# Optimization experiments

Measured on AMD Instinct MI355X. Metric: run time of the kernel, lower is better.

## Reference

```python
import jax, jax.numpy as jnp
import numpy as np

N_NODES = 100000
N_EDGES = 1280000
D_IN = 64
D_HID = 128
D_OUT = 64


def sage_conv(x, src, dst, W_l, b_l, W_r, n_nodes):
    # PyG SAGEConv (aggr='mean', root_weight=True):
    #   out_i = W_l @ mean_{j in N(i)} x_j + b_l + W_r @ x_i
    msg = x[src]  # [E, d] gather of source-node features
    agg = jax.ops.segment_sum(msg, dst, num_segments=n_nodes)  # [N, d]
    cnt = jax.ops.segment_sum(jnp.ones((src.shape[0], 1), x.dtype), dst,
                              num_segments=n_nodes)  # [N, 1]
    mean = agg / jnp.maximum(cnt, 1.0)  # zero-neighbor nodes -> 0 (matches scatter-mean)
    return mean @ W_l.T + b_l + x @ W_r.T


def setup_inputs() -> dict:
    key = jax.random.key(0)
    ks = jax.random.split(key, 8)
    x = jax.random.normal(ks[0], (N_NODES, D_IN), dtype=jnp.float32)
    edge_index = jax.random.randint(ks[1], (2, N_EDGES), 0, N_NODES, dtype=jnp.int64)
    s = 0.05
    W_l1 = jax.random.normal(ks[2], (D_HID, D_IN), dtype=jnp.float32) * s
    b_l1 = jnp.zeros((D_HID,), dtype=jnp.float32)
    W_r1 = jax.random.normal(ks[3], (D_HID, D_IN), dtype=jnp.float32) * s
    W_l2 = jax.random.normal(ks[4], (D_OUT, D_HID), dtype=jnp.float32) * s
    b_l2 = jnp.zeros((D_OUT,), dtype=jnp.float32)
    W_r2 = jax.random.normal(ks[5], (D_OUT, D_HID), dtype=jnp.float32) * s
    return {"x": x, "edge_index": edge_index,
            "W_l1": W_l1, "b_l1": b_l1, "W_r1": W_r1,
            "W_l2": W_l2, "b_l2": b_l2, "W_r2": W_r2}


def reference(x, edge_index, W_l1, b_l1, W_r1, W_l2, b_l2, W_r2):
    src, dst = edge_index[0], edge_index[1]
    n = x.shape[0]
    h = sage_conv(x, src, dst, W_l1, b_l1, W_r1, n)
    h = jax.nn.relu(h)
    out = sage_conv(h, src, dst, W_l2, b_l2, W_r2, n)
    return out
```

## Files before the change

kernel.cpp:

```cpp
#include <hip/hip_runtime.h>
#include <cstdint>
#include <cstddef>

typedef __attribute__((ext_vector_type(8))) short short8;
typedef __attribute__((ext_vector_type(4))) float floatx4;

static constexpr int DIN  = 64;
static constexpr int DHID = 128;
static constexpr int BSH  = 7;
static constexpr int BNODES = 1 << BSH;
static constexpr int TILE = 8192;
static constexpr int CAP  = 4096;
static constexpr unsigned SENT = 0xFFFFFFFFu;

__device__ inline short f2bf(float f) {
  unsigned u = __float_as_uint(f);
  u += 0x7FFF + ((u >> 16) & 1);
  return (short)(u >> 16);
}
__device__ inline float bf2f(short s) {
  return __uint_as_float(((unsigned)(unsigned short)s) << 16);
}

__global__ __launch_bounds__(64) void detect_kernel(const void* edges, int E, long long nmax, int* mode) {
  const long long* e64 = (const long long*)edges;
  int lane = threadIdx.x;
  int nchk = E < 256 ? E : 256;
  bool ok = true;
  for (int i = lane; i < nchk; i += 64) {
    long long v = e64[i];
    if (v < 0 || v >= nmax) ok = false;
  }
  unsigned long long b = __ballot(ok);
  if (lane == 0) *mode = (b == ~0ull) ? 1 : 0;
}

__global__ __launch_bounds__(256) void prep_kernel(const float* __restrict__ x,
    const float* __restrict__ Wl1, const float* __restrict__ Wr1,
    const float* __restrict__ Wl2, const float* __restrict__ Wr2,
    short* __restrict__ xb, short* __restrict__ wc1, short* __restrict__ wc2,
    int nx, int gx)
{
  int b = blockIdx.x, t = threadIdx.x;
  if (b < gx) {
    int i0 = (b * 256 + t) * 8;
    if (i0 < nx) {
      floatx4 f0 = *(const floatx4*)&x[i0];
      floatx4 f1 = *(const floatx4*)&x[i0 + 4];
      short8 o;
      o[0]=f2bf(f0[0]); o[1]=f2bf(f0[1]); o[2]=f2bf(f0[2]); o[3]=f2bf(f0[3]);
      o[4]=f2bf(f1[0]); o[5]=f2bf(f1[1]); o[6]=f2bf(f1[2]); o[7]=f2bf(f1[3]);
      *(short8*)&xb[i0] = o;
    }
  } else {
    int wb = b - gx;
    int idx = ((wb & 15) * 256 + t) * 4;
    int n = idx >> 7, k = idx & 127;
    const float* src;
    if (wb < 16) src = (k < 64) ? &Wl1[n * 64 + k] : &Wr1[n * 64 + (k - 64)];
    else         src = (n < 64) ? &Wl2[n * 128 + k] : &Wr2[(n - 64) * 128 + k];
    floatx4 f = *(const floatx4*)src;
    short* dst = (wb < 16 ? wc1 : wc2) + idx;
    dst[0]=f2bf(f[0]); dst[1]=f2bf(f[1]); dst[2]=f2bf(f[2]); dst[3]=f2bf(f[3]);
  }
}

__global__ __launch_bounds__(256) void partition_kernel(const void* edges, const int* __restrict__ mode,
                                                        int* __restrict__ bucket_cursor,
                                                        int* __restrict__ real_cnt,
                                                        unsigned* __restrict__ packed, int E, int NB) {
  __shared__ unsigned sval[TILE];
  __shared__ unsigned saux[TILE];
  __shared__ int hist[1024];
  __shared__ int gb[1024];
  int t = threadIdx.x;
  int base = blockIdx.x * TILE;
  int cnt_here = E - base; if (cnt_here > TILE) cnt_here = TILE;
  for (int i = t; i < NB; i += 256) hist[i] = 0;
  __syncthreads();
  bool m64 = (*mode != 0);
  #pragma unroll 4
  for (int c = 0; c < TILE / 256; ++c) {
    int idx = c * 256 + t;
    if (idx < cnt_here) {
      int i = base + idx;
      int s, d;
      if (m64) { const long long* e = (const long long*)edges; s = (int)e[i]; d = (int)e[(size_t)E + i]; }
      else     { const int*       e = (const int*)edges;       s = e[i];      d = e[(size_t)E + i]; }
      int b = d >> BSH;
      int rank = atomicAdd(&hist[b], 1);
      sval[idx] = ((unsigned)(d & (BNODES - 1)) << 17) | (unsigned)s;
      saux[idx] = ((unsigned)b << 13) | (unsigned)rank;
    }
  }
  __syncthreads();
  for (int b = t; b < NB; b += 256) {
    int cnt = hist[b];
    int gbase = 0;
    if (cnt > 0) {
      int pad = (cnt + 15) & ~15;
      gbase = b * CAP + atomicAdd(&bucket_cursor[b], pad);
      atomicAdd(&real_cnt[b], cnt);
      for (int j = cnt; j < pad; ++j) packed[gbase + j] = SENT;
    }
    gb[b] = gbase;
  }
  __syncthreads();
  #pragma unroll 4
  for (int c = 0; c < TILE / 256; ++c) {
    int idx = c * 256 + t;
    if (idx < cnt_here) {
      unsigned a = saux[idx];
      packed[gb[a >> 13] + (a & 0x1FFFu)] = sval[idx];
    }
  }
}

__global__ __launch_bounds__(256) void bucket_scan_kernel(const int* __restrict__ real_cnt,
                                                          int* __restrict__ ebase,
                                                          int* __restrict__ row_ptr,
                                                          int NB, int N, int E) {
  int t = threadIdx.x;
  int i0 = t * 4;
  int v[4]; int s = 0;
  #pragma unroll
  for (int c = 0; c < 4; ++c) { int idx = i0 + c; v[c] = (idx < NB) ? real_cnt[idx] : 0; s += v[c]; }
  int lane = t & 63, w = t >> 6;
  int val = s;
  #pragma unroll
  for (int off = 1; off < 64; off <<= 1) {
    int u = __shfl_up(val, off, 64);
    if (lane >= off) val += u;
  }
  __shared__ int wsum[4];
  if (lane == 63) wsum[w] = val;
  __syncthreads();
  int wpre = 0;
  for (int ww = 0; ww < w; ++ww) wpre += wsum[ww];
  int run = wpre + val - s;
  #pragma unroll
  for (int c = 0; c < 4; ++c) { int idx = i0 + c; if (idx < NB) ebase[idx] = run; run += v[c]; }
  if (t == 0) row_ptr[N] = E;
}

__global__ __launch_bounds__(256) void bucket_sort_kernel(const unsigned* __restrict__ packed,
                                                          const int* __restrict__ bucket_cursor,
                                                          const int* __restrict__ ebase,
                                                          int* __restrict__ row_ptr,
                                                          int* __restrict__ sorted_src, int N) {
  __shared__ int nhist[BNODES];
  __shared__ int cur[BNODES];
  __shared__ int wsum[4];
  int b = blockIdx.x, t = threadIdx.x;
  int n0 = b << BSH;
  int nn = N - n0; if (nn > BNODES) nn = BNODES;
  if (t < BNODES) nhist[t] = 0;
  __syncthreads();
  int rbeg = b * CAP, rcnt = bucket_cursor[b];
  for (int i = t; i < rcnt; i += 256) {
    unsigned p = packed[rbeg + i];
    if (p != SENT) atomicAdd(&nhist[p >> 17], 1);
  }
  __syncthreads();
  int lane = t & 63, w = t >> 6;
  int v = (t < BNODES) ? nhist[t] : 0;
  int val = v;
  #pragma unroll
  for (int off = 1; off < 64; off <<= 1) {
    int u = __shfl_up(val, off, 64);
    if (lane >= off) val += u;
  }
  if (lane == 63) wsum[w] = val;
  __syncthreads();
  int pre = (w == 1) ? wsum[0] : 0;
  int excl = pre + val - v;
  int eb = ebase[b];
  if (t < nn) { row_ptr[n0 + t] = eb + excl; cur[t] = eb + excl; }
  __syncthreads();
  for (int i = t; i < rcnt; i += 256) {
    unsigned p = packed[rbeg + i];
    if (p != SENT) {
      int pos = atomicAdd(&cur[p >> 17], 1);
      sorted_src[pos] = (int)(p & 0x1FFFFu);
    }
  }
}

template <bool EPI>
__global__ __launch_bounds__(256) void agg_bf16_kernel(const short* __restrict__ feat,
                                                       const int* __restrict__ row_ptr,
                                                       const int* __restrict__ srcs,
                                                       const float* __restrict__ rbuf,
                                                       const float* __restrict__ bias,
                                                       short* __restrict__ outb,
                                                       float* __restrict__ outf, int N) {
  int node = blockIdx.x * 32 + (threadIdx.x >> 3);
  if (node >= N) return;
  int c = threadIdx.x & 7;
  const short* fbase = feat + c * 8;
  int beg = row_ptr[node], end = row_ptr[node + 1];
  float acc[8];
  #pragma unroll
  for (int j = 0; j < 8; ++j) acc[j] = 0.f;
  int e = beg;
  for (; e + 4 <= end; e += 4) {
    int s0 = srcs[e], s1 = srcs[e + 1], s2 = srcs[e + 2], s3 = srcs[e + 3];
    short8 v0 = *(const short8*)&fbase[(size_t)s0 * 64];
    short8 v1 = *(const short8*)&fbase[(size_t)s1 * 64];
    short8 v2 = *(const short8*)&fbase[(size_t)s2 * 64];
    short8 v3 = *(const short8*)&fbase[(size_t)s3 * 64];
    #pragma unroll
    for (int j = 0; j < 8; ++j)
      acc[j] += (bf2f(v0[j]) + bf2f(v1[j])) + (bf2f(v2[j]) + bf2f(v3[j]));
  }
  for (; e < end; ++e) {
    short8 v = *(const short8*)&fbase[(size_t)srcs[e] * 64];
    #pragma unroll
    for (int j = 0; j < 8; ++j) acc[j] += bf2f(v[j]);
  }
  float inv = 1.f / fmaxf((float)(end - beg), 1.f);
  if (!EPI) {
    short8 o;
    #pragma unroll
    for (int j = 0; j < 8; ++j) o[j] = f2bf(acc[j] * inv);
    *(short8*)&outb[(size_t)node * 64 + c * 8] = o;
  } else {
    floatx4 b0 = *(const floatx4*)&bias[c * 8];
    floatx4 b1 = *(const floatx4*)&bias[c * 8 + 4];
    floatx4 r0 = *(const floatx4*)&rbuf[(size_t)node * 64 + c * 8];
    floatx4 r1 = *(const floatx4*)&rbuf[(size_t)node * 64 + c * 8 + 4];
    floatx4 o0, o1;
    #pragma unroll
    for (int j = 0; j < 4; ++j) {
      o0[j] = acc[j] * inv + b0[j] + r0[j];
      o1[j] = acc[4 + j] * inv + b1[j] + r1[j];
    }
    *(floatx4*)&outf[(size_t)node * 64 + c * 8]     = o0;
    *(floatx4*)&outf[(size_t)node * 64 + c * 8 + 4] = o1;
  }
}

template <int MODE>
__global__ __launch_bounds__(256) void mfma_gemm_kernel(
    const short* __restrict__ Aa, const short* __restrict__ Ab, int lda,
    const short* __restrict__ Wcat, const float* __restrict__ bias,
    short* __restrict__ Cb, float* __restrict__ Cf, int M)
{
  __shared__ short Ws[128][136];
  int t = threadIdx.x;
  #pragma unroll
  for (int i = 0; i < 8; ++i) {
    int idx = i * 256 + t;
    int r = idx >> 4, c8 = (idx & 15) * 8;
    *(short8*)&Ws[r][c8] = *(const short8*)&Wcat[r * 128 + c8];
  }
  __syncthreads();
  int wv = t >> 6, lane = t & 63, q = lane >> 4, l15 = lane & 15;
  int m0 = blockIdx.x * 64 + wv * 16;
  int row = m0 + l15;
  bool rowok = row < M;
  floatx4 acc[8];
  #pragma unroll
  for (int nt = 0; nt < 8; ++nt) acc[nt] = (floatx4){0.f, 0.f, 0.f, 0.f};
  #pragma unroll
  for (int ko = 0; ko < 4; ++ko) {
    const short* Asrc = (ko < 2) ? Aa : Ab;
    short8 a = {0, 0, 0, 0, 0, 0, 0, 0};
    if (rowok) a = *(const short8*)&Asrc[(size_t)row * lda + (ko & 1) * 32 + q * 8];
    #pragma unroll
    for (int nt = 0; nt < 8; ++nt) {
      short8 b = *(const short8*)&Ws[nt * 16 + l15][ko * 32 + q * 8];
      acc[nt] = __builtin_amdgcn_mfma_f32_16x16x32_bf16(a, b, acc[nt], 0, 0, 0);
    }
  }
  #pragma unroll
  for (int nt = 0; nt < 8; ++nt) {
    int n = nt * 16 + l15;
    float bv = (MODE == 0) ? bias[n] : 0.f;
    #pragma unroll
    for (int r2 = 0; r2 < 4; ++r2) {
      int mr = m0 + q * 4 + r2;
      if (mr >= M) continue;
      float v = acc[nt][r2] + bv;
      if (MODE == 0) {
        v = fmaxf(v, 0.f);
        Cb[(size_t)mr * 128 + n] = f2bf(v);
      } else {
        if (nt < 4) Cb[(size_t)mr * 64 + n] = f2bf(v);
        else        Cf[(size_t)mr * 64 + (n - 64)] = v;
      }
    }
  }
}

extern "C" void kernel_launch(void* const* d_in, const int* in_sizes, int n_in,
                              void* d_out, int out_size, void* d_ws, size_t ws_size,
                              hipStream_t stream) {
  const float* x   = (const float*)d_in[0];
  const void*  ei  = d_in[1];
  const float* Wl1 = (const float*)d_in[2];
  const float* bl1 = (const float*)d_in[3];
  const float* Wr1 = (const float*)d_in[4];
  const float* Wl2 = (const float*)d_in[5];
  const float* bl2 = (const float*)d_in[6];
  const float* Wr2 = (const float*)d_in[7];
  int N = in_sizes[0] / DIN;
  int E = in_sizes[1] / 2;
  int NB = (N + BNODES - 1) / BNODES;

  char* w = (char*)d_ws;
  size_t off = 0;
  auto alloc = [&](size_t bytes) -> void* {
    void* p = w + off;
    off += (bytes + 255) & ~(size_t)255;
    return p;
  };
  int*      mode       = (int*)alloc(16);
  int*      bcur       = (int*)alloc((size_t)NB * 8);
  int*      rcnt       = bcur + NB;
  int*      ebase      = (int*)alloc((size_t)NB * 4);
  int*      row_ptr    = (int*)alloc(((size_t)N + 1) * 4);
  unsigned* packed     = (unsigned*)alloc((size_t)NB * CAP * 4);
  int*      sorted_src = (int*)alloc((size_t)E * 4);
  short*    xb         = (short*)alloc((size_t)N * 64 * 2);
  short*    meanb      = (short*)alloc((size_t)N * 64 * 2);
  short*    h          = (short*)alloc((size_t)N * DHID * 2);
  float*    rbuf       = (float*)alloc((size_t)N * 64 * 4);
  short*    wc1        = (short*)alloc(128 * 128 * 2);
  short*    wc2        = (short*)alloc(128 * 128 * 2);
  (void)ws_size; (void)n_in; (void)out_size;

  hipMemsetAsync(bcur, 0, (size_t)NB * 8, stream);
  detect_kernel<<<1, 64, 0, stream>>>(ei, E, (long long)N, mode);

  int nx = N * DIN;
  int gx = (nx / 8 + 255) / 256;
  prep_kernel<<<gx + 32, 256, 0, stream>>>(x, Wl1, Wr1, Wl2, Wr2, xb, wc1, wc2, nx, gx);

  int gP = (E + TILE - 1) / TILE;
  partition_kernel<<<gP, 256, 0, stream>>>(ei, mode, bcur, rcnt, packed, E, NB);
  bucket_scan_kernel<<<1, 256, 0, stream>>>(rcnt, ebase, row_ptr, NB, N, E);
  bucket_sort_kernel<<<NB, 256, 0, stream>>>(packed, bcur, ebase, row_ptr, sorted_src, N);

  int gN32 = (N + 31) / 32;
  agg_bf16_kernel<false><<<gN32, 256, 0, stream>>>(xb, row_ptr, sorted_src, nullptr, nullptr, meanb, nullptr, N);

  int gm = (N + 63) / 64;
  mfma_gemm_kernel<0><<<gm, 256, 0, stream>>>(meanb, xb, 64, wc1, bl1, h, nullptr, N);
  mfma_gemm_kernel<1><<<gm, 256, 0, stream>>>(h, h + 64, 128, wc2, nullptr, meanb, rbuf, N);

  agg_bf16_kernel<true><<<gN32, 256, 0, stream>>>(meanb, row_ptr, sorted_src, rbuf, bl2, nullptr, (float*)d_out, N);
}
```

Baseline: 222.2 us.

## Fuse both node GEMMs via LDS and fold memset/detect into other kernels

The two MFMA GEMM launches are merged into one kernel. The ReLU'd hidden tile stays in shared memory and feeds the second GEMM directly, so the N×128 bf16 hidden buffer is never written to or read back from global memory. The bucket-cursor memset moves into extra blocks of the prep kernel, and the int64/int32 edge-format check moves into every partition block, removing two small launches. The cost is more LDS per block (second weight load plus the H tile), a redundant format check in each partition block, and the second GEMM's output writing over meanb in place.

Result: faster. 207.4 us (-6.7%).

```diff
diff --git a/kernel.cpp b/kernel.cpp
--- a/kernel.cpp
+++ b/kernel.cpp
@@ -22,23 +22,11 @@
   return __uint_as_float(((unsigned)(unsigned short)s) << 16);
 }
 
-__global__ __launch_bounds__(64) void detect_kernel(const void* edges, int E, long long nmax, int* mode) {
-  const long long* e64 = (const long long*)edges;
-  int lane = threadIdx.x;
-  int nchk = E < 256 ? E : 256;
-  bool ok = true;
-  for (int i = lane; i < nchk; i += 64) {
-    long long v = e64[i];
-    if (v < 0 || v >= nmax) ok = false;
-  }
-  unsigned long long b = __ballot(ok);
-  if (lane == 0) *mode = (b == ~0ull) ? 1 : 0;
-}
-
 __global__ __launch_bounds__(256) void prep_kernel(const float* __restrict__ x,
     const float* __restrict__ Wl1, const float* __restrict__ Wr1,
     const float* __restrict__ Wl2, const float* __restrict__ Wr2,
     short* __restrict__ xb, short* __restrict__ wc1, short* __restrict__ wc2,
+    int* __restrict__ bcur, int nz,
     int nx, int gx)
 {
   int b = blockIdx.x, t = threadIdx.x;
@@ -52,7 +40,7 @@
       o[4]=f2bf(f1[0]); o[5]=f2bf(f1[1]); o[6]=f2bf(f1[2]); o[7]=f2bf(f1[3]);
       *(short8*)&xb[i0] = o;
     }
-  } else {
+  } else if (b < gx + 32) {
     int wb = b - gx;
     int idx = ((wb & 15) * 256 + t) * 4;
     int n = idx >> 7, k = idx & 127;
@@ -62,10 +50,12 @@
     floatx4 f = *(const floatx4*)src;
     short* dst = (wb < 16 ? wc1 : wc2) + idx;
     dst[0]=f2bf(f[0]); dst[1]=f2bf(f[1]); dst[2]=f2bf(f[2]); dst[3]=f2bf(f[3]);
-  }
-}
-
-__global__ __launch_bounds__(256) void partition_kernel(const void* edges, const int* __restrict__ mode,
+  } else {
+    for (int i = t; i < nz; i += 256) bcur[i] = 0;
+  }
+}
+
+__global__ __launch_bounds__(256) void partition_kernel(const void* edges, long long nmax,
                                                         int* __restrict__ bucket_cursor,
                                                         int* __restrict__ real_cnt,
                                                         unsigned* __restrict__ packed, int E, int NB) {
@@ -73,12 +63,25 @@
   __shared__ unsigned saux[TILE];
   __shared__ int hist[1024];
   __shared__ int gb[1024];
+  __shared__ int smode;
   int t = threadIdx.x;
   int base = blockIdx.x * TILE;
   int cnt_here = E - base; if (cnt_here > TILE) cnt_here = TILE;
   for (int i = t; i < NB; i += 256) hist[i] = 0;
-  __syncthreads();
-  bool m64 = (*mode != 0);
+  if (t == 0) smode = 1;
+  __syncthreads();
+  {
+    const long long* e64 = (const long long*)edges;
+    int nchk = E < 256 ? E : 256;
+    bool ok = true;
+    for (int i = t; i < nchk; i += 256) {
+      long long v = e64[i];
+      if (v < 0 || v >= nmax) ok = false;
+    }
+    if (!ok) smode = 0;
+  }
+  __syncthreads();
+  bool m64 = (smode != 0);
   #pragma unroll 4
   for (int c = 0; c < TILE / 256; ++c) {
     int idx = c * 256 + t;
@@ -240,19 +243,20 @@
   }
 }
 
-template <int MODE>
-__global__ __launch_bounds__(256) void mfma_gemm_kernel(
-    const short* __restrict__ Aa, const short* __restrict__ Ab, int lda,
-    const short* __restrict__ Wcat, const float* __restrict__ bias,
-    short* __restrict__ Cb, float* __restrict__ Cf, int M)
+__global__ __launch_bounds__(256) void fused_gemm_kernel(
+    const short* __restrict__ Aa, const short* __restrict__ Ab,
+    const short* __restrict__ wc1, const short* __restrict__ wc2,
+    const float* __restrict__ bias1,
+    short* __restrict__ Cg, float* __restrict__ Cr, int M)
 {
   __shared__ short Ws[128][136];
+  __shared__ short Hs[64][136];
   int t = threadIdx.x;
   #pragma unroll
   for (int i = 0; i < 8; ++i) {
     int idx = i * 256 + t;
     int r = idx >> 4, c8 = (idx & 15) * 8;
-    *(short8*)&Ws[r][c8] = *(const short8*)&Wcat[r * 128 + c8];
+    *(short8*)&Ws[r][c8] = *(const short8*)&wc1[r * 128 + c8];
   }
   __syncthreads();
   int wv = t >> 6, lane = t & 63, q = lane >> 4, l15 = lane & 15;
@@ -266,7 +270,7 @@
   for (int ko = 0; ko < 4; ++ko) {
     const short* Asrc = (ko < 2) ? Aa : Ab;
     short8 a = {0, 0, 0, 0, 0, 0, 0, 0};
-    if (rowok) a = *(const short8*)&Asrc[(size_t)row * lda + (ko & 1) * 32 + q * 8];
+    if (rowok) a = *(const short8*)&Asrc[(size_t)row * 64 + (ko & 1) * 32 + q * 8];
     #pragma unroll
     for (int nt = 0; nt < 8; ++nt) {
       short8 b = *(const short8*)&Ws[nt * 16 + l15][ko * 32 + q * 8];
@@ -276,19 +280,43 @@
   #pragma unroll
   for (int nt = 0; nt < 8; ++nt) {
     int n = nt * 16 + l15;
-    float bv = (MODE == 0) ? bias[n] : 0.f;
+    float bv = bias1[n];
+    #pragma unroll
+    for (int r2 = 0; r2 < 4; ++r2) {
+      int lr = wv * 16 + q * 4 + r2;
+      float v = fmaxf(acc[nt][r2] + bv, 0.f);
+      Hs[lr][n] = f2bf(v);
+    }
+  }
+  __syncthreads();
+  #pragma unroll
+  for (int i = 0; i < 8; ++i) {
+    int idx = i * 256 + t;
+    int r = idx >> 4, c8 = (idx & 15) * 8;
+    *(short8*)&Ws[r][c8] = *(const short8*)&wc2[r * 128 + c8];
+  }
+  __syncthreads();
+  #pragma unroll
+  for (int nt = 0; nt < 8; ++nt) acc[nt] = (floatx4){0.f, 0.f, 0.f, 0.f};
+  #pragma unroll
+  for (int ko = 0; ko < 4; ++ko) {
+    short8 a = *(const short8*)&Hs[wv * 16 + l15][ko * 32 + q * 8];
+    #pragma unroll
+    for (int nt = 0; nt < 8; ++nt) {
+      short8 b = *(const short8*)&Ws[nt * 16 + l15][ko * 32 + q * 8];
+      acc[nt] = __builtin_amdgcn_mfma_f32_16x16x32_bf16(a, b, acc[nt], 0, 0, 0);
+    }
+  }
+  #pragma unroll
+  for (int nt = 0; nt < 8; ++nt) {
+    int n = nt * 16 + l15;
     #pragma unroll
     for (int r2 = 0; r2 < 4; ++r2) {
       int mr = m0 + q * 4 + r2;
       if (mr >= M) continue;
-      float v = acc[nt][r2] + bv;
-      if (MODE == 0) {
-        v = fmaxf(v, 0.f);
-        Cb[(size_t)mr * 128 + n] = f2bf(v);
-      } else {
-        if (nt < 4) Cb[(size_t)mr * 64 + n] = f2bf(v);
-        else        Cf[(size_t)mr * 64 + (n - 64)] = v;
-      }
+      float v = acc[nt][r2];
+      if (nt < 4) Cg[(size_t)mr * 64 + n] = f2bf(v);
+      else        Cr[(size_t)mr * 64 + (n - 64)] = v;
     }
   }
 }
@@ -315,7 +343,6 @@
     off += (bytes + 255) & ~(size_t)255;
     return p;
   };
-  int*      mode       = (int*)alloc(16);
   int*      bcur       = (int*)alloc((size_t)NB * 8);
   int*      rcnt       = bcur + NB;
   int*      ebase      = (int*)alloc((size_t)NB * 4);
@@ -324,21 +351,18 @@
   int*      sorted_src = (int*)alloc((size_t)E * 4);
   short*    xb         = (short*)alloc((size_t)N * 64 * 2);
   short*    meanb      = (short*)alloc((size_t)N * 64 * 2);
-  short*    h          = (short*)alloc((size_t)N * DHID * 2);
   float*    rbuf       = (float*)alloc((size_t)N * 64 * 4);
   short*    wc1        = (short*)alloc(128 * 128 * 2);
   short*    wc2        = (short*)alloc(128 * 128 * 2);
   (void)ws_size; (void)n_in; (void)out_size;
 
-  hipMemsetAsync(bcur, 0, (size_t)NB * 8, stream);
-  detect_kernel<<<1, 64, 0, stream>>>(ei, E, (long long)N, mode);
-
   int nx = N * DIN;
   int gx = (nx / 8 + 255) / 256;
-  prep_kernel<<<gx + 32, 256, 0, stream>>>(x, Wl1, Wr1, Wl2, Wr2, xb, wc1, wc2, nx, gx);
+  prep_kernel<<<gx + 33, 256, 0, stream>>>(x, Wl1, Wr1, Wl2, Wr2, xb, wc1, wc2,
+                                           bcur, NB * 2, nx, gx);
 
   int gP = (E + TILE - 1) / TILE;
-  partition_kernel<<<gP, 256, 0, stream>>>(ei, mode, bcur, rcnt, packed, E, NB);
+  partition_kernel<<<gP, 256, 0, stream>>>(ei, (long long)N, bcur, rcnt, packed, E, NB);
   bucket_scan_kernel<<<1, 256, 0, stream>>>(rcnt, ebase, row_ptr, NB, N, E);
   bucket_sort_kernel<<<NB, 256, 0, stream>>>(packed, bcur, ebase, row_ptr, sorted_src, N);
 
@@ -346,8 +370,7 @@
   agg_bf16_kernel<false><<<gN32, 256, 0, stream>>>(xb, row_ptr, sorted_src, nullptr, nullptr, meanb, nullptr, N);
 
   int gm = (N + 63) / 64;
-  mfma_gemm_kernel<0><<<gm, 256, 0, stream>>>(meanb, xb, 64, wc1, bl1, h, nullptr, N);
-  mfma_gemm_kernel<1><<<gm, 256, 0, stream>>>(h, h + 64, 128, wc2, nullptr, meanb, rbuf, N);
+  fused_gemm_kernel<<<gm, 256, 0, stream>>>(meanb, xb, wc1, wc2, bl1, meanb, rbuf, N);
 
   agg_bf16_kernel<true><<<gN32, 256, 0, stream>>>(meanb, row_ptr, sorted_src, rbuf, bl2, nullptr, (float*)d_out, N);
 }
```
